# Optimization experiments

Measured on AMD Instinct MI355X. Metric: run time of the kernel, lower is better.

## Reference

```python
import jax, jax.numpy as jnp
import numpy as np

B, NA, NB, E = 2, 256, 256, 512
H1, H2 = 300, 100


def setup_inputs() -> dict:
    key = jax.random.key(0)
    ks = jax.random.split(key, 16)

    def n(k, shape, scale=1.0):
        return jax.random.normal(k, shape, dtype=jnp.float32) * scale

    z = lambda shape: jnp.zeros(shape, jnp.float32)
    return {
        "action_embedding": n(ks[0], (B, E, NA)),
        "anchor_embedding": n(ks[1], (B, E, NB)),
        "action_points": n(ks[2], (B, 3, NA)),
        "anchor_points": n(ks[3], (B, 3, NB)),
        # pairwise MLP kernel params: 2E -> 300 -> 100 -> 1
        "mlp_W1": n(ks[4], (2 * E, H1), (2 * E) ** -0.5),
        "mlp_b1": z((H1,)),
        "mlp_W2": n(ks[5], (H1, H2), H1 ** -0.5),
        "mlp_b2": z((H2,)),
        "mlp_W3": n(ks[6], (H2, 1), H2 ** -0.5),
        "mlp_b3": z((1,)),
        # PointNet [512,64,64,64,128,512] (1x1 convs) + Conv1d(512,1,bias=False)
        "pn_W0": n(ks[7], (64, 512), 512 ** -0.5),
        "pn_b0": z((64,)),
        "pn_W1": n(ks[8], (64, 64), 64 ** -0.5),
        "pn_b1": z((64,)),
        "pn_W2": n(ks[9], (64, 64), 64 ** -0.5),
        "pn_b2": z((64,)),
        "pn_W3": n(ks[10], (128, 64), 64 ** -0.5),
        "pn_b3": z((128,)),
        "pn_W4": n(ks[11], (512, 128), 128 ** -0.5),
        "pn_b4": z((512,)),
        "head_W": n(ks[12], (1, 512), 512 ** -0.5),
    }


def reference(action_embedding, anchor_embedding, action_points, anchor_points,
              mlp_W1, mlp_b1, mlp_W2, mlp_b2, mlp_W3, mlp_b3,
              pn_W0, pn_b0, pn_W1, pn_b1, pn_W2, pn_b2, pn_W3, pn_b3,
              pn_W4, pn_b4, head_W):
    P_A = action_points.transpose(0, 2, 1)      # (B, NA, 3)
    P_B = anchor_points.transpose(0, 2, 1)      # (B, NB, 3)
    Phi_A = action_embedding.transpose(0, 2, 1)  # (B, NA, E)
    Phi_B = anchor_embedding.transpose(0, 2, 1)  # (B, NB, E)
    Ed = Phi_A.shape[-1]

    # --- symmetric pairwise MLP kernel: softplus((mlp(cat(a,b)) + mlp(cat(b,a))) / 2) ---
    # First Linear layer is split so the O(NA*NB*2E) concat is never materialized:
    # cat(a,b) @ W1 == a @ W1[:E] + b @ W1[E:]
    W1a, W1b = mlp_W1[:Ed], mlp_W1[Ed:]

    def mlp_tail(h):  # h: (B, NA, NB, H1) pre-activation of layer 1
        h = jax.nn.relu(h)
        h = jax.nn.relu(h @ mlp_W2 + mlp_b2)
        return (h @ mlp_W3 + mlp_b3)[..., 0]  # (B, NA, NB)

    hA_a = Phi_A @ W1a  # (B, NA, H1)
    hA_b = Phi_A @ W1b
    hB_a = Phi_B @ W1a  # (B, NB, H1)
    hB_b = Phi_B @ W1b
    v1 = mlp_tail(hA_a[:, :, None, :] + hB_b[:, None, :, :] + mlp_b1)  # mlp(cat(x1,x2))
    v2 = mlp_tail(hB_a[:, None, :, :] + hA_b[:, :, None, :] + mlp_b1)  # mlp(cat(x2,x1))
    R_est = jax.nn.softplus((v1 + v2) * 0.5)  # (B, NA, NB) estimated distances

    # --- weighted multilateration (estimate_p), vectorized over (B, NA) ---
    # Linearized LS: ||p||^2 - 2 q_k^T p = r_k^2 - ||q_k||^2; subtract weighted means
    # to eliminate ||p||^2, then solve 3x3 weighted normal equations per action point.
    w = jnp.ones(P_B.shape[:2], R_est.dtype)            # (B, NB) uniform weights (last_attn=False)
    wsum = w.sum(-1, keepdims=True)                      # (B, 1)
    qbar = (w[..., None] * P_B).sum(1) / wsum            # (B, 3)
    bvec = (P_B ** 2).sum(-1)[:, None, :] - R_est ** 2   # (B, NA, NB)
    bbar = (w[:, None, :] * bvec).sum(-1) / wsum         # (B, NA)
    Amat = 2.0 * (P_B - qbar[:, None, :])                # (B, NB, 3)
    yvec = bvec - bbar[..., None]                        # (B, NA, NB)
    M = jnp.einsum('bki,bk,bkj->bij', Amat, w, Amat)     # (B, 3, 3)
    rhs = jnp.einsum('bki,bk,bak->bai', Amat, w, yvec)   # (B, NA, 3)
    P_A_B_pred = jnp.linalg.solve(M[:, None], rhs[..., None])[..., 0]  # (B, NA, 3)

    flow = (P_A_B_pred - P_A).transpose(0, 2, 1)         # (B, 3, NA)

    # --- PointNet flow-weight head (1x1 convs + ReLU, final conv no bias) ---
    x = action_embedding                                  # (B, 512, NA)
    for Wc, bc in ((pn_W0, pn_b0), (pn_W1, pn_b1), (pn_W2, pn_b2),
                   (pn_W3, pn_b3), (pn_W4, pn_b4)):
        x = jax.nn.relu(jnp.einsum('oi,bin->bon', Wc, x) + bc[None, :, None])
    weight = jnp.einsum('oi,bin->bon', head_W, x)        # (B, 1, NA)

    full_flow = jnp.concatenate([flow, weight], axis=1)  # (B, 4, NA)
    return full_flow
```

## Files before the change

kernel.cpp:

```cpp
#include <hip/hip_runtime.h>
#include <hip/hip_bf16.h>
#include <hip/hip_fp16.h>

typedef float f32x4 __attribute__((ext_vector_type(4)));
typedef short s16x8 __attribute__((ext_vector_type(8)));
typedef _Float16 f16x8 __attribute__((ext_vector_type(8)));

#define OFF_EMBT   0u
#define OFF_W1T    1048576u
#define OFF_W2TSW  1662976u
#define OFF_W0BF   1734656u
#define OFF_HA     1800192u
#define OFF_R2     3110912u
#define WS_TOTAL   3635200u

__device__ __forceinline__ int pack_bf2(float a, float b) {
  __hip_bfloat162 h = __float22bfloat162_rn(make_float2(a, b));
  int r; __builtin_memcpy(&r, &h, 4); return r;
}
__device__ __forceinline__ unsigned pack_f16_2(float a, float b) {
  __half2 h = __float22half2_rn(make_float2(a, b));
  unsigned r; __builtin_memcpy(&r, &h, 4); return r;
}
__device__ __forceinline__ unsigned short bf16u(float f) {
  __hip_bfloat16 h = __float2bfloat16(f);
  unsigned short u; __builtin_memcpy(&u, &h, 2); return u;
}
__device__ __forceinline__ s16x8 i4_to_s8(int a, int b, int c, int d) {
  union { int i[4]; s16x8 s; } u;
  u.i[0] = a; u.i[1] = b; u.i[2] = c; u.i[3] = d; return u.s;
}

__global__ __launch_bounds__(256) void ka_prep(
    const float* __restrict__ act_emb, const float* __restrict__ anc_emb,
    const float* __restrict__ W1, const float* __restrict__ W2,
    const float* __restrict__ W0pn, char* __restrict__ ws)
{
  __hip_bfloat16* embT  = (__hip_bfloat16*)(ws + OFF_EMBT);
  __hip_bfloat16* W1T   = (__hip_bfloat16*)(ws + OFF_W1T);
  unsigned short* W2Tsw = (unsigned short*)(ws + OFF_W2TSW);
  unsigned short* W0bf  = (unsigned short*)(ws + OFF_W0BF);
  __shared__ float tile[64][65];
  int blk = blockIdx.x, t = threadIdx.x;
  if (blk < 128) {
    int b = blk >> 6, emb = (blk >> 5) & 1, ntile = (blk >> 3) & 3, etile = blk & 7;
    const float* src = emb ? anc_emb : act_emb;
    int e0 = etile * 64, n0 = ntile * 64;
    int rr = t >> 6, cc = t & 63;
    #pragma unroll
    for (int it2 = 0; it2 < 16; ++it2) {
      int e_l = rr * 16 + it2;
      tile[e_l][cc] = src[(size_t)(b * 512 + e0 + e_l) * 256 + n0 + cc];
    }
    __syncthreads();
    int n_l = t >> 2, eq = t & 3;
    unsigned int* dst = (unsigned int*)(embT + ((size_t)((b * 2 + emb) * 256 + n0 + n_l)) * 512 + e0 + eq * 16);
    #pragma unroll
    for (int kk = 0; kk < 8; ++kk)
      dst[kk] = (unsigned)pack_bf2(tile[eq * 16 + 2 * kk][n_l], tile[eq * 16 + 2 * kk + 1][n_l]);
  } else if (blk < 208) {
    int id = blk - 128;
    int half = id / 40; int rem = id % 40; int et = rem / 5; int ct = rem % 5;
    int e0 = et * 64, c0 = ct * 64;
    int rr = t >> 6, cc = t & 63;
    #pragma unroll
    for (int it2 = 0; it2 < 16; ++it2) {
      int e_l = rr * 16 + it2;
      int c = c0 + cc;
      tile[e_l][cc] = (c < 300) ? W1[(size_t)(half * 512 + e0 + e_l) * 300 + c] : 0.f;
    }
    __syncthreads();
    int c_l = t >> 2, eq = t & 3;
    if (c0 + c_l < 300) {
      unsigned int* dst = (unsigned int*)(W1T + ((size_t)(half * 300 + c0 + c_l)) * 512 + e0 + eq * 16);
      #pragma unroll
      for (int kk = 0; kk < 8; ++kk)
        dst[kk] = (unsigned)pack_bf2(tile[eq * 16 + 2 * kk][c_l], tile[eq * 16 + 2 * kk + 1][c_l]);
    }
  } else if (blk < 226) {
    int idx = (blk - 208) * 256 + t;
    if (idx < 4480) {
      int unit = idx >> 6; int lane = idx & 63;
      int ks = unit / 7; int nt = unit - ks * 7;
      int n = nt * 16 + (lane & 15);
      int kb = ks * 32 + (lane >> 4) * 8;
      unsigned int q[4];
      #pragma unroll
      for (int jj = 0; jj < 4; ++jj) {
        int k0 = kb + jj * 2, k1 = kb + jj * 2 + 1;
        float f0 = (n < 100 && k0 < 300) ? W2[(size_t)k0 * 100 + n] : 0.f;
        float f1 = (n < 100 && k1 < 300) ? W2[(size_t)k1 * 100 + n] : 0.f;
        q[jj] = pack_f16_2(f0, f1);
      }
      ((uint4*)W2Tsw)[idx] = make_uint4(q[0], q[1], q[2], q[3]);
    }
  } else if (blk < 242) {
    int idx = (blk - 226) * 256 + t;
    const float* s = W0pn + (size_t)idx * 8;
    ((uint4*)W0bf)[idx] = make_uint4(
        (unsigned)pack_bf2(s[0], s[1]), (unsigned)pack_bf2(s[2], s[3]),
        (unsigned)pack_bf2(s[4], s[5]), (unsigned)pack_bf2(s[6], s[7]));
  } else {
    int idx = (blk - 242) * 256 + t;
    _Float16* ha = (_Float16*)(ws + OFF_HA);
    #pragma unroll
    for (int rr = 0; rr < 2; ++rr) {
      int row = idx * 2 + rr;
      unsigned* p = (unsigned*)(ha + (size_t)row * 320 + 300);
      #pragma unroll
      for (int q2 = 0; q2 < 10; ++q2) p[q2] = 0u;
    }
  }
}

template<int K, int NT>
__device__ __forceinline__ void pn_layer(unsigned short* xb, const float* __restrict__ W,
                                         const float* __restrict__ bias, int wv, int l, int g)
{
  constexpr int NN = NT / 4;
  f32x4 z = {0.f, 0.f, 0.f, 0.f};
  f32x4 acc[NN];
  #pragma unroll
  for (int nn = 0; nn < NN; ++nn) acc[nn] = z;
  #pragma unroll
  for (int nn = 0; nn < NN; ++nn) {
    int o = (wv + nn * 4) * 16 + l;
    const float* wr0 = W + (size_t)o * K;
    #pragma unroll
    for (int ks = 0; ks < K / 32; ++ks) {
      int koff = ks * 32 + g * 8;
      f32x4 wa = *(const f32x4*)(wr0 + koff);
      f32x4 wb = *(const f32x4*)(wr0 + koff + 4);
      s16x8 bfr = i4_to_s8(pack_bf2(wa.x, wa.y), pack_bf2(wa.z, wa.w),
                           pack_bf2(wb.x, wb.y), pack_bf2(wb.z, wb.w));
      s16x8 a0 = *(const s16x8*)(xb + (size_t)l * 520 + koff);
      acc[nn] = __builtin_amdgcn_mfma_f32_16x16x32_bf16(a0, bfr, acc[nn], 0, 0, 0);
    }
  }
  __syncthreads();
  #pragma unroll
  for (int nn = 0; nn < NN; ++nn) {
    int chan = (wv + nn * 4) * 16 + l;
    float bv = bias[chan];
    #pragma unroll
    for (int r = 0; r < 4; ++r)
      xb[(size_t)(g * 4 + r) * 520 + chan] = bf16u(fmaxf(acc[nn][r] + bv, 0.f));
  }
  __syncthreads();
}

__global__ __launch_bounds__(256) void k1_ha(
    const __hip_bfloat16* __restrict__ embT, const __hip_bfloat16* __restrict__ W1T,
    const float* __restrict__ b1, _Float16* __restrict__ ha_ws,
    const unsigned short* __restrict__ W0bf,
    const float* __restrict__ pnW1, const float* __restrict__ pnW2,
    const float* __restrict__ pnW3, const float* __restrict__ pnW4,
    const float* __restrict__ pnB0, const float* __restrict__ pnB1,
    const float* __restrict__ pnB2, const float* __restrict__ pnB3,
    const float* __restrict__ pnB4,
    const float* __restrict__ headW, float* __restrict__ out)
{
  __shared__ unsigned short xbuf[16 * 520];
  int blk = blockIdx.x, t = threadIdx.x;
  int wv = t >> 6, lane = t & 63, l = lane & 15, g = lane >> 4;
  if (blk < 320) {
    int b = blk / 160; int r = blk % 160; int emb = r / 80; r %= 80;
    int mch = r / 5; int nch = r % 5;
    int m0 = mch * 16;
    const unsigned short* Ap = (const unsigned short*)embT +
        ((size_t)((b * 2 + emb) * 256 + m0 + l)) * 512;
    const unsigned short* Wp = (const unsigned short*)W1T;
    f32x4 z = {0.f, 0.f, 0.f, 0.f};
    f32x4 acc[2] = {z, z};
    for (int ks = 0; ks < 16; ++ks) {
      int k0 = ks * 32 + g * 8;
      s16x8 af = *(const s16x8*)(Ap + k0);
      #pragma unroll
      for (int q = 0; q < 2; ++q) {
        int c = nch * 120 + (wv * 2 + q) * 16 + l;
        s16x8 bf = {0, 0, 0, 0, 0, 0, 0, 0};
        if (c < 600) bf = *(const s16x8*)(Wp + (size_t)c * 512 + k0);
        acc[q] = __builtin_amdgcn_mfma_f32_16x16x32_bf16(af, bf, acc[q], 0, 0, 0);
      }
    }
    #pragma unroll
    for (int q = 0; q < 2; ++q) {
      int cl = (wv * 2 + q) * 16 + l;
      int c = nch * 120 + cl;
      if (cl < 120 && c < 600) {
        int half = (c >= 300) ? 1 : 0;
        int cc = c - half * 300;
        float bias = (emb == 0) ? b1[cc] : 0.f;
        _Float16* Dp = ha_ws + ((size_t)((b * 4 + emb * 2 + half) * 256 + m0 + g * 4)) * 320 + cc;
        #pragma unroll
        for (int r2 = 0; r2 < 4; ++r2)
          Dp[(size_t)r2 * 320] = (_Float16)__float2half_rn(acc[q][r2] + bias);
      }
    }
  } else {
    int pn = blk - 320;
    int b_pn = pn >> 4, n0 = (pn & 15) * 16;
    unsigned short* xb = xbuf;
    {
      const unsigned short* A0 = (const unsigned short*)embT + ((size_t)(b_pn * 2 * 256 + n0)) * 512;
      f32x4 acc0 = {0.f, 0.f, 0.f, 0.f};
      int o = wv * 16 + l;
      const unsigned short* w0r = W0bf + (size_t)o * 512;
      #pragma unroll
      for (int ks = 0; ks < 16; ++ks) {
        int koff = ks * 32 + g * 8;
        s16x8 bfr = *(const s16x8*)(w0r + koff);
        s16x8 a0 = *(const s16x8*)(A0 + (size_t)l * 512 + koff);
        acc0 = __builtin_amdgcn_mfma_f32_16x16x32_bf16(a0, bfr, acc0, 0, 0, 0);
      }
      float bv = pnB0[o];
      #pragma unroll
      for (int r2 = 0; r2 < 4; ++r2)
        xb[(size_t)(g * 4 + r2) * 520 + o] = bf16u(fmaxf(acc0[r2] + bv, 0.f));
      __syncthreads();
    }
    pn_layer<64, 4>(xb, pnW1, pnB1, wv, l, g);
    pn_layer<64, 4>(xb, pnW2, pnB2, wv, l, g);
    pn_layer<64, 8>(xb, pnW3, pnB3, wv, l, g);
    pn_layer<128, 32>(xb, pnW4, pnB4, wv, l, g);
    {
      int p_l = t >> 4, os = t & 15;
      const unsigned short* row = xb + (size_t)p_l * 520 + os * 32;
      float s = 0.f;
      #pragma unroll
      for (int c = 0; c < 32; ++c) {
        unsigned int u = ((unsigned int)row[c]) << 16;
        float xv; __builtin_memcpy(&xv, &u, 4);
        s += xv * headW[os * 32 + c];
      }
      s += __shfl_xor(s, 1); s += __shfl_xor(s, 2);
      s += __shfl_xor(s, 4); s += __shfl_xor(s, 8);
      if (os == 0) out[(size_t)(b_pn * 4 + 3) * 256 + n0 + p_l] = s;
    }
  }
}

__global__ __launch_bounds__(1024, 8) void k2_main(
    const _Float16* __restrict__ ha_ws, const unsigned short* __restrict__ W2Tsw,
    const float* __restrict__ b2g, const float* __restrict__ W3g, const float* __restrict__ b3g,
    float* __restrict__ R2)
{
  __shared__ int4 w2s[4480];
  __shared__ float pvbuf[128];
  int blk = blockIdx.x, t = threadIdx.x;
  int wv = t >> 6, lane = t & 63, l = lane & 15, g = lane >> 4;
  int rep = wv >> 3, jw = wv & 7;
  int b = blk >> 9, it = (blk >> 5) & 15, jt = blk & 31;
  int i0 = it * 16, j = jt * 8 + jw;
  {
    const int4* w2g = (const int4*)W2Tsw;
    for (int u = t; u < 4480; u += 1024) w2s[u] = w2g[u];
  }
  __syncthreads();
  const _Float16* hap = ha_ws + ((size_t)((b * 4 + rep) * 256 + i0 + l)) * 320 + g * 8;
  const _Float16* hbp = ha_ws + ((size_t)((b * 4 + (rep ? 2 : 3)) * 256 + j)) * 320 + g * 8;
  f32x4 z = {0.f, 0.f, 0.f, 0.f};
  f32x4 acc[7];
  #pragma unroll
  for (int nt = 0; nt < 7; ++nt) acc[nt] = z;
  const f16x8 zf = {0, 0, 0, 0, 0, 0, 0, 0};
  #pragma unroll
  for (int ks = 0; ks < 10; ++ks) {
    f16x8 ha = *(const f16x8*)(hap + ks * 32);
    f16x8 hb = *(const f16x8*)(hbp + ks * 32);
    f16x8 af = __builtin_elementwise_max(ha + hb, zf);
    const int4* wp = &w2s[ks * 448 + lane];
    #pragma unroll
    for (int nt = 0; nt < 7; ++nt) {
      f16x8 bf = *(const f16x8*)(wp + nt * 64);
      acc[nt] = __builtin_amdgcn_mfma_f32_16x16x32_f16(af, bf, acc[nt], 0, 0, 0);
    }
  }
  float pv[4];
  {
    float w3v[7], b2v[7];
    #pragma unroll
    for (int nt = 0; nt < 7; ++nt) {
      int n = nt * 16 + l;
      w3v[nt] = (n < 100) ? W3g[n] : 0.f;
      b2v[nt] = (n < 100) ? b2g[n] : 0.f;
    }
    #pragma unroll
    for (int r = 0; r < 4; ++r) {
      float p = 0.f;
      #pragma unroll
      for (int nt = 0; nt < 7; ++nt)
        p += fmaxf(acc[nt][r] + b2v[nt], 0.f) * w3v[nt];
      p += __shfl_xor(p, 1);
      p += __shfl_xor(p, 2);
      p += __shfl_xor(p, 4);
      p += __shfl_xor(p, 8);
      pv[r] = p;
    }
  }
  if (rep == 1 && l == 0) {
    #pragma unroll
    for (int r = 0; r < 4; ++r) pvbuf[jw * 16 + g * 4 + r] = pv[r];
  }
  __syncthreads();
  if (rep == 0 && l == 0) {
    float b3 = b3g[0];
    #pragma unroll
    for (int r = 0; r < 4; ++r) {
      float S = 0.5f * (pv[r] + pvbuf[jw * 16 + g * 4 + r]) + b3;
      float Rr = (S > 20.f) ? S : log1pf(expf(S));
      R2[((size_t)(b * 256 + i0 + g * 4 + r)) * 256 + j] = Rr * Rr;
    }
  }
}

__device__ __forceinline__ float block_sum(float v, float* redbuf, int t) {
  #pragma unroll
  for (int m = 1; m < 64; m <<= 1) v += __shfl_xor(v, m);
  __syncthreads();
  if ((t & 63) == 0) redbuf[t >> 6] = v;
  __syncthreads();
  return redbuf[0] + redbuf[1] + redbuf[2] + redbuf[3];
}

__global__ __launch_bounds__(256) void k3_solve(
    const float* __restrict__ anc_pts, const float* __restrict__ act_pts,
    const float* __restrict__ R2, float* __restrict__ out)
{
  __shared__ float Ax[256], Ay[256], Az[256];
  __shared__ float redbuf[4];
  int blk = blockIdx.x, t = threadIdx.x;
  int b = blk >> 2, ic = blk & 3;
  int k = t;
  float px = anc_pts[(size_t)(b * 3 + 0) * 256 + k];
  float py = anc_pts[(size_t)(b * 3 + 1) * 256 + k];
  float pz = anc_pts[(size_t)(b * 3 + 2) * 256 + k];
  float qx = block_sum(px, redbuf, t) * (1.f / 256.f);
  float qy = block_sum(py, redbuf, t) * (1.f / 256.f);
  float qz = block_sum(pz, redbuf, t) * (1.f / 256.f);
  float ax = 2.f * (px - qx), ay = 2.f * (py - qy), az = 2.f * (pz - qz);
  float p2 = px * px + py * py + pz * pz;
  Ax[k] = ax; Ay[k] = ay; Az[k] = az;
  float mxx = block_sum(ax * ax, redbuf, t);
  float mxy = block_sum(ax * ay, redbuf, t);
  float mxz = block_sum(ax * az, redbuf, t);
  float myy = block_sum(ay * ay, redbuf, t);
  float myz = block_sum(ay * az, redbuf, t);
  float mzz = block_sum(az * az, redbuf, t);
  float c0x = block_sum(ax * p2, redbuf, t);
  float c0y = block_sum(ay * p2, redbuf, t);
  float c0z = block_sum(az * p2, redbuf, t);
  __syncthreads();
  float det = mxx * (myy * mzz - myz * myz) - mxy * (mxy * mzz - myz * mxz) + mxz * (mxy * myz - myy * mxz);
  float idet = 1.f / det;
  float i00 = (myy * mzz - myz * myz) * idet;
  float i01 = (mxz * myz - mxy * mzz) * idet;
  float i02 = (mxy * myz - mxz * myy) * idet;
  float i11 = (mxx * mzz - mxz * mxz) * idet;
  float i12 = (mxy * mxz - mxx * myz) * idet;
  float i22 = (mxx * myy - mxy * mxy) * idet;
  int il = t >> 2, ks = t & 3;
  int i = ic * 64 + il;
  const float* rrow = R2 + ((size_t)(b * 256 + i)) * 256;
  float r0 = 0.f, r1 = 0.f, r2 = 0.f;
  #pragma unroll
  for (int kk = 0; kk < 16; ++kk) {
    int kb = ks * 64 + kk * 4;
    f32x4 rv = *(const f32x4*)(rrow + kb);
    r0 += Ax[kb] * rv.x + Ax[kb + 1] * rv.y + Ax[kb + 2] * rv.z + Ax[kb + 3] * rv.w;
    r1 += Ay[kb] * rv.x + Ay[kb + 1] * rv.y + Ay[kb + 2] * rv.z + Ay[kb + 3] * rv.w;
    r2 += Az[kb] * rv.x + Az[kb + 1] * rv.y + Az[kb + 2] * rv.z + Az[kb + 3] * rv.w;
  }
  r0 += __shfl_xor(r0, 1); r0 += __shfl_xor(r0, 2);
  r1 += __shfl_xor(r1, 1); r1 += __shfl_xor(r1, 2);
  r2 += __shfl_xor(r2, 1); r2 += __shfl_xor(r2, 2);
  if (ks == 0) {
    float hx = c0x - r0, hy = c0y - r1, hz = c0z - r2;
    float x0 = i00 * hx + i01 * hy + i02 * hz;
    float x1 = i01 * hx + i11 * hy + i12 * hz;
    float x2 = i02 * hx + i12 * hy + i22 * hz;
    out[(size_t)(b * 4 + 0) * 256 + i] = x0 - act_pts[(size_t)(b * 3 + 0) * 256 + i];
    out[(size_t)(b * 4 + 1) * 256 + i] = x1 - act_pts[(size_t)(b * 3 + 1) * 256 + i];
    out[(size_t)(b * 4 + 2) * 256 + i] = x2 - act_pts[(size_t)(b * 3 + 2) * 256 + i];
  }
}

extern "C" void kernel_launch(void* const* d_in, const int* in_sizes, int n_in,
                              void* d_out, int out_size, void* d_ws, size_t ws_size,
                              hipStream_t stream)
{
  const float* act_emb = (const float*)d_in[0];
  const float* anc_emb = (const float*)d_in[1];
  const float* act_pts = (const float*)d_in[2];
  const float* anc_pts = (const float*)d_in[3];
  const float* W1  = (const float*)d_in[4];
  const float* b1  = (const float*)d_in[5];
  const float* W2  = (const float*)d_in[6];
  const float* b2  = (const float*)d_in[7];
  const float* W3  = (const float*)d_in[8];
  const float* b3  = (const float*)d_in[9];
  const float* pnW0 = (const float*)d_in[10];
  const float* pnB0 = (const float*)d_in[11];
  const float* pnW1 = (const float*)d_in[12];
  const float* pnB1 = (const float*)d_in[13];
  const float* pnW2 = (const float*)d_in[14];
  const float* pnB2 = (const float*)d_in[15];
  const float* pnW3 = (const float*)d_in[16];
  const float* pnB3 = (const float*)d_in[17];
  const float* pnW4 = (const float*)d_in[18];
  const float* pnB4 = (const float*)d_in[19];
  const float* headW = (const float*)d_in[20];
  char* ws = (char*)d_ws;
  __hip_bfloat16* embT  = (__hip_bfloat16*)(ws + OFF_EMBT);
  __hip_bfloat16* W1T   = (__hip_bfloat16*)(ws + OFF_W1T);
  unsigned short* W2Tsw = (unsigned short*)(ws + OFF_W2TSW);
  unsigned short* W0bf  = (unsigned short*)(ws + OFF_W0BF);
  _Float16* ha_ws = (_Float16*)(ws + OFF_HA);
  float* R2ws  = (float*)(ws + OFF_R2);
  float* outp  = (float*)d_out;

  ka_prep<<<246, 256, 0, stream>>>(act_emb, anc_emb, W1, W2, pnW0, ws);
  k1_ha<<<352, 256, 0, stream>>>(embT, W1T, b1, ha_ws, W0bf,
                                 pnW1, pnW2, pnW3, pnW4, pnB0, pnB1, pnB2, pnB3, pnB4,
                                 headW, outp);
  k2_main<<<1024, 1024, 0, stream>>>(ha_ws, W2Tsw, b2, W3, b3, R2ws);
  k3_solve<<<8, 256, 0, stream>>>(anc_pts, act_pts, R2ws, outp);
}
```

Measured before the change: 168.8 us.

## Switch pairwise MLP layer-2 to 32x32x16 MFMA with 32-row tiles

The second MLP layer in k2_main now uses 32x32x16 f16 MFMA instead of 16x16x32, with each block covering 32 action rows rather than 16. The grid is halved and the W2 swizzle layout in the prep kernel changes to match. The N padding drops from 112 to 128 columns but now needs only 4 MFMA tiles, and each W2 fragment from LDS is reused over more rows, so fewer LDS reads and instructions are issued per output. In exchange, the 16-float accumulators per tile raise register pressure (launch bounds go from 8 to 4), and the extra padded columns add some wasted compute.

Measured after the change: 182.4 us. 8.0% more time.

```diff
diff --git a/kernel.cpp b/kernel.cpp
--- a/kernel.cpp
+++ b/kernel.cpp
@@ -3,16 +3,17 @@
 #include <hip/hip_fp16.h>
 
 typedef float f32x4 __attribute__((ext_vector_type(4)));
+typedef float f32x16 __attribute__((ext_vector_type(16)));
 typedef short s16x8 __attribute__((ext_vector_type(8)));
 typedef _Float16 f16x8 __attribute__((ext_vector_type(8)));
 
 #define OFF_EMBT   0u
 #define OFF_W1T    1048576u
 #define OFF_W2TSW  1662976u
-#define OFF_W0BF   1734656u
-#define OFF_HA     1800192u
-#define OFF_R2     3110912u
-#define WS_TOTAL   3635200u
+#define OFF_W0BF   1744896u
+#define OFF_HA     1810432u
+#define OFF_R2     3121152u
+#define WS_TOTAL   3645440u
 
 __device__ __forceinline__ int pack_bf2(float a, float b) {
   __hip_bfloat162 h = __float22bfloat162_rn(make_float2(a, b));
@@ -77,31 +78,29 @@
       for (int kk = 0; kk < 8; ++kk)
         dst[kk] = (unsigned)pack_bf2(tile[eq * 16 + 2 * kk][c_l], tile[eq * 16 + 2 * kk + 1][c_l]);
     }
-  } else if (blk < 226) {
+  } else if (blk < 228) {
     int idx = (blk - 208) * 256 + t;
-    if (idx < 4480) {
-      int unit = idx >> 6; int lane = idx & 63;
-      int ks = unit / 7; int nt = unit - ks * 7;
-      int n = nt * 16 + (lane & 15);
-      int kb = ks * 32 + (lane >> 4) * 8;
-      unsigned int q[4];
-      #pragma unroll
-      for (int jj = 0; jj < 4; ++jj) {
-        int k0 = kb + jj * 2, k1 = kb + jj * 2 + 1;
-        float f0 = (n < 100 && k0 < 300) ? W2[(size_t)k0 * 100 + n] : 0.f;
-        float f1 = (n < 100 && k1 < 300) ? W2[(size_t)k1 * 100 + n] : 0.f;
-        q[jj] = pack_f16_2(f0, f1);
-      }
-      ((uint4*)W2Tsw)[idx] = make_uint4(q[0], q[1], q[2], q[3]);
-    }
-  } else if (blk < 242) {
-    int idx = (blk - 226) * 256 + t;
+    int unit = idx >> 6; int lane = idx & 63;
+    int ks = unit >> 2; int nt = unit & 3;
+    int n = nt * 32 + (lane & 31);
+    int kb = ks * 16 + (lane >> 5) * 8;
+    unsigned int q[4];
+    #pragma unroll
+    for (int jj = 0; jj < 4; ++jj) {
+      int k0 = kb + jj * 2, k1 = kb + jj * 2 + 1;
+      float f0 = (n < 100 && k0 < 300) ? W2[(size_t)k0 * 100 + n] : 0.f;
+      float f1 = (n < 100 && k1 < 300) ? W2[(size_t)k1 * 100 + n] : 0.f;
+      q[jj] = pack_f16_2(f0, f1);
+    }
+    ((uint4*)W2Tsw)[idx] = make_uint4(q[0], q[1], q[2], q[3]);
+  } else if (blk < 244) {
+    int idx = (blk - 228) * 256 + t;
     const float* s = W0pn + (size_t)idx * 8;
     ((uint4*)W0bf)[idx] = make_uint4(
         (unsigned)pack_bf2(s[0], s[1]), (unsigned)pack_bf2(s[2], s[3]),
         (unsigned)pack_bf2(s[4], s[5]), (unsigned)pack_bf2(s[6], s[7]));
   } else {
-    int idx = (blk - 242) * 256 + t;
+    int idx = (blk - 244) * 256 + t;
     _Float16* ha = (_Float16*)(ws + OFF_HA);
     #pragma unroll
     for (int rr = 0; rr < 2; ++rr) {
@@ -240,76 +239,84 @@
   }
 }
 
-__global__ __launch_bounds__(1024, 8) void k2_main(
+__global__ __launch_bounds__(1024, 4) void k2_main(
     const _Float16* __restrict__ ha_ws, const unsigned short* __restrict__ W2Tsw,
     const float* __restrict__ b2g, const float* __restrict__ W3g, const float* __restrict__ b3g,
     float* __restrict__ R2)
 {
-  __shared__ int4 w2s[4480];
-  __shared__ float pvbuf[128];
+  __shared__ union { int4 w2s[5120]; float pvbuf[256]; } sm;
   int blk = blockIdx.x, t = threadIdx.x;
-  int wv = t >> 6, lane = t & 63, l = lane & 15, g = lane >> 4;
+  int wv = t >> 6, lane = t & 63;
+  int m = lane & 31, h = lane >> 5;
   int rep = wv >> 3, jw = wv & 7;
-  int b = blk >> 9, it = (blk >> 5) & 15, jt = blk & 31;
-  int i0 = it * 16, j = jt * 8 + jw;
+  int b = blk >> 8, it = (blk >> 5) & 7, jt = blk & 31;
+  int i0 = it * 32, j = jt * 8 + jw;
   {
     const int4* w2g = (const int4*)W2Tsw;
-    for (int u = t; u < 4480; u += 1024) w2s[u] = w2g[u];
-  }
-  __syncthreads();
-  const _Float16* hap = ha_ws + ((size_t)((b * 4 + rep) * 256 + i0 + l)) * 320 + g * 8;
-  const _Float16* hbp = ha_ws + ((size_t)((b * 4 + (rep ? 2 : 3)) * 256 + j)) * 320 + g * 8;
-  f32x4 z = {0.f, 0.f, 0.f, 0.f};
-  f32x4 acc[7];
-  #pragma unroll
-  for (int nt = 0; nt < 7; ++nt) acc[nt] = z;
+    #pragma unroll
+    for (int u = 0; u < 5; ++u) sm.w2s[t + u * 1024] = w2g[t + u * 1024];
+  }
+  __syncthreads();
+  const _Float16* hap = ha_ws + ((size_t)((b * 4 + rep) * 256 + i0 + m)) * 320 + h * 8;
+  const _Float16* hbp = ha_ws + ((size_t)((b * 4 + (rep ? 2 : 3)) * 256 + j)) * 320 + h * 8;
+  f32x16 acc[4];
+  #pragma unroll
+  for (int nt = 0; nt < 4; ++nt)
+    #pragma unroll
+    for (int r = 0; r < 16; ++r) acc[nt][r] = 0.f;
   const f16x8 zf = {0, 0, 0, 0, 0, 0, 0, 0};
   #pragma unroll
-  for (int ks = 0; ks < 10; ++ks) {
-    f16x8 ha = *(const f16x8*)(hap + ks * 32);
-    f16x8 hb = *(const f16x8*)(hbp + ks * 32);
+  for (int ks = 0; ks < 20; ++ks) {
+    f16x8 ha = *(const f16x8*)(hap + ks * 16);
+    f16x8 hb = *(const f16x8*)(hbp + ks * 16);
     f16x8 af = __builtin_elementwise_max(ha + hb, zf);
-    const int4* wp = &w2s[ks * 448 + lane];
-    #pragma unroll
-    for (int nt = 0; nt < 7; ++nt) {
+    const int4* wp = &sm.w2s[ks * 256 + lane];
+    #pragma unroll
+    for (int nt = 0; nt < 4; ++nt) {
       f16x8 bf = *(const f16x8*)(wp + nt * 64);
-      acc[nt] = __builtin_amdgcn_mfma_f32_16x16x32_f16(af, bf, acc[nt], 0, 0, 0);
-    }
-  }
-  float pv[4];
+      acc[nt] = __builtin_amdgcn_mfma_f32_32x32x16_f16(af, bf, acc[nt], 0, 0, 0);
+    }
+  }
+  float pv[16];
   {
-    float w3v[7], b2v[7];
-    #pragma unroll
-    for (int nt = 0; nt < 7; ++nt) {
-      int n = nt * 16 + l;
+    float w3v[4], b2v[4];
+    #pragma unroll
+    for (int nt = 0; nt < 4; ++nt) {
+      int n = nt * 32 + m;
       w3v[nt] = (n < 100) ? W3g[n] : 0.f;
       b2v[nt] = (n < 100) ? b2g[n] : 0.f;
     }
     #pragma unroll
-    for (int r = 0; r < 4; ++r) {
+    for (int r = 0; r < 16; ++r) {
       float p = 0.f;
       #pragma unroll
-      for (int nt = 0; nt < 7; ++nt)
+      for (int nt = 0; nt < 4; ++nt)
         p += fmaxf(acc[nt][r] + b2v[nt], 0.f) * w3v[nt];
       p += __shfl_xor(p, 1);
       p += __shfl_xor(p, 2);
       p += __shfl_xor(p, 4);
       p += __shfl_xor(p, 8);
+      p += __shfl_xor(p, 16);
       pv[r] = p;
     }
   }
-  if (rep == 1 && l == 0) {
-    #pragma unroll
-    for (int r = 0; r < 4; ++r) pvbuf[jw * 16 + g * 4 + r] = pv[r];
-  }
-  __syncthreads();
-  if (rep == 0 && l == 0) {
+  __syncthreads();
+  if (rep == 1 && m == 0) {
+    #pragma unroll
+    for (int r = 0; r < 16; ++r) {
+      int il = (r & 3) + 8 * (r >> 2) + 4 * h;
+      sm.pvbuf[jw * 32 + il] = pv[r];
+    }
+  }
+  __syncthreads();
+  if (rep == 0 && m == 0) {
     float b3 = b3g[0];
     #pragma unroll
-    for (int r = 0; r < 4; ++r) {
-      float S = 0.5f * (pv[r] + pvbuf[jw * 16 + g * 4 + r]) + b3;
+    for (int r = 0; r < 16; ++r) {
+      int il = (r & 3) + 8 * (r >> 2) + 4 * h;
+      float S = 0.5f * (pv[r] + sm.pvbuf[jw * 32 + il]) + b3;
       float Rr = (S > 20.f) ? S : log1pf(expf(S));
-      R2[((size_t)(b * 256 + i0 + g * 4 + r)) * 256 + j] = Rr * Rr;
+      R2[((size_t)(b * 256 + i0 + il)) * 256 + j] = Rr * Rr;
     }
   }
 }
@@ -419,10 +426,10 @@
   float* R2ws  = (float*)(ws + OFF_R2);
   float* outp  = (float*)d_out;
 
-  ka_prep<<<246, 256, 0, stream>>>(act_emb, anc_emb, W1, W2, pnW0, ws);
+  ka_prep<<<248, 256, 0, stream>>>(act_emb, anc_emb, W1, W2, pnW0, ws);
   k1_ha<<<352, 256, 0, stream>>>(embT, W1T, b1, ha_ws, W0bf,
                                  pnW1, pnW2, pnW3, pnW4, pnB0, pnB1, pnB2, pnB3, pnB4,
                                  headW, outp);
-  k2_main<<<1024, 1024, 0, stream>>>(ha_ws, W2Tsw, b2, W3, b3, R2ws);
+  k2_main<<<512, 1024, 0, stream>>>(ha_ws, W2Tsw, b2, W3, b3, R2ws);
   k3_solve<<<8, 256, 0, stream>>>(anc_pts, act_pts, R2ws, outp);
 }
```
